# Performance work log

Hardware: AMD Instinct MI355X
Metric: run time of the kernel (lower is better)

The kernel has to match this reference:

```python
import jax, jax.numpy as jnp
import numpy as np

HIDDEN = 1024
HEADS = 16
HEAD_DIM = HIDDEN // HEADS


def setup_inputs() -> dict:
    key = jax.random.key(0)
    kx, kq, kk, kv, ko = jax.random.split(key, 5)
    s = 1.0 / np.sqrt(HIDDEN)
    return {
        "x": jax.random.normal(kx, (2, 2048, HIDDEN), dtype=jnp.float32),
        # nn.Linear weights, stored [out, in] like torch
        "Wq": jax.random.uniform(kq, (HIDDEN, HIDDEN), jnp.float32, -s, s),
        "Wk": jax.random.uniform(kk, (HIDDEN, HIDDEN), jnp.float32, -s, s),
        "Wv": jax.random.uniform(kv, (HIDDEN, HIDDEN), jnp.float32, -s, s),
        "Wo": jax.random.uniform(ko, (HIDDEN, HIDDEN), jnp.float32, -s, s),
    }


def reference(x, Wq, Wk, Wv, Wo):
    B, S, D = x.shape
    H, Hd = HEADS, HEAD_DIM

    def proj(W):  # torch Linear: x @ W.T -> [B,H,S,Hd]
        return (x @ W.T).reshape(B, S, H, Hd).transpose(0, 2, 1, 3)

    q, k, v = proj(Wq), proj(Wk), proj(Wv)
    scores = jnp.einsum("bhsd,bhtd->bhst", q, k) / max(Hd ** 0.5, 1e-6)
    causal = jnp.tril(jnp.ones((S, S), dtype=bool))  # True = keep
    scores = jnp.where(causal, scores, -jnp.inf)
    attn = jax.nn.softmax(scores, axis=-1)
    y = jnp.einsum("bhst,bhtd->bhsd", attn, v)
    y = y.transpose(0, 2, 1, 3).reshape(B, S, D)
    return y @ Wo.T
```

## Files before the change

### kernel.cpp

```cpp
#include <hip/hip_runtime.h>
#include <hip/hip_bf16.h>


#define S_LEN  2048
#define BATCH  2
#define DMODEL 1024
#define NHEADS 16
#define HDIM   64

typedef short short8 __attribute__((ext_vector_type(8)));
typedef float f32x4  __attribute__((ext_vector_type(4)));

__device__ __forceinline__ float b2f(unsigned short u) {
    union { unsigned int i; float f; } x; x.i = ((unsigned int)u) << 16; return x.f;
}
__device__ __forceinline__ unsigned short f2b(float f) {
    union { float f; unsigned int i; } x; x.f = f;
    unsigned int r = x.i + 0x7fffu + ((x.i >> 16) & 1u);
    return (unsigned short)(r >> 16);
}

__device__ __forceinline__ unsigned short* swzp(unsigned short* base, int row, int col) {
    int byte = (col << 1) ^ ((((row >> 3) ^ row) & 7) << 4);
    return base + (row << 6) + (byte >> 1);
}

__global__ void cast_kernel(const float* __restrict__ in, unsigned short* __restrict__ out, int n4) {
    int i = blockIdx.x * blockDim.x + threadIdx.x;
    if (i >= n4) return;
    float4 v = ((const float4*)in)[i];
    unsigned int lo = (unsigned int)f2b(v.x) | ((unsigned int)f2b(v.y) << 16);
    unsigned int hi = (unsigned int)f2b(v.z) | ((unsigned int)f2b(v.w) << 16);
    ((uint2*)out)[i] = make_uint2(lo, hi);
}

template<int OUT_BF16>
__global__ __launch_bounds__(256) void gemm_nt(const unsigned short* __restrict__ A,
                                               const unsigned short* __restrict__ W,
                                               unsigned short* __restrict__ Cb,
                                               float* __restrict__ Cf,
                                               int M, int N, int K) {
    (void)M;
    __shared__ unsigned short As[64][80];
    __shared__ unsigned short Bs[64][80];
    const int tid  = threadIdx.x;
    const int lane = tid & 63;
    const int wave = tid >> 6;
    const int bm = blockIdx.y * 64;
    const int bn = blockIdx.x * 64;
    const int wr = (wave >> 1) * 32;
    const int wc = (wave & 1) * 32;
    const int l15 = lane & 15;
    const int l4  = lane >> 4;
    const int srow = tid >> 2;
    const int sk   = (tid & 3) * 16;

    f32x4 acc[2][2];
#pragma unroll
    for (int i = 0; i < 2; ++i)
#pragma unroll
        for (int j = 0; j < 2; ++j) acc[i][j] = (f32x4){0.f,0.f,0.f,0.f};

    const unsigned short* Arow = A + (size_t)(bm + srow) * K + sk;
    const unsigned short* Wrow = W + (size_t)(bn + srow) * K + sk;

    for (int k0 = 0; k0 < K; k0 += 64) {
        uint4 a0 = *(const uint4*)(Arow + k0);
        uint4 a1 = *(const uint4*)(Arow + k0 + 8);
        uint4 b0 = *(const uint4*)(Wrow + k0);
        uint4 b1 = *(const uint4*)(Wrow + k0 + 8);
        __syncthreads();
        *(uint4*)&As[srow][sk]     = a0;
        *(uint4*)&As[srow][sk + 8] = a1;
        *(uint4*)&Bs[srow][sk]     = b0;
        *(uint4*)&Bs[srow][sk + 8] = b1;
        __syncthreads();
#pragma unroll
        for (int kk = 0; kk < 2; ++kk) {
            short8 af0 = *(const short8*)&As[wr + l15]     [kk*32 + l4*8];
            short8 af1 = *(const short8*)&As[wr + 16 + l15][kk*32 + l4*8];
            short8 bf0 = *(const short8*)&Bs[wc + l15]     [kk*32 + l4*8];
            short8 bf1 = *(const short8*)&Bs[wc + 16 + l15][kk*32 + l4*8];
            acc[0][0] = __builtin_amdgcn_mfma_f32_16x16x32_bf16(af0, bf0, acc[0][0], 0, 0, 0);
            acc[0][1] = __builtin_amdgcn_mfma_f32_16x16x32_bf16(af0, bf1, acc[0][1], 0, 0, 0);
            acc[1][0] = __builtin_amdgcn_mfma_f32_16x16x32_bf16(af1, bf0, acc[1][0], 0, 0, 0);
            acc[1][1] = __builtin_amdgcn_mfma_f32_16x16x32_bf16(af1, bf1, acc[1][1], 0, 0, 0);
        }
    }
#pragma unroll
    for (int mi = 0; mi < 2; ++mi)
#pragma unroll
        for (int ni = 0; ni < 2; ++ni)
#pragma unroll
            for (int i = 0; i < 4; ++i) {
                int row = bm + wr + mi*16 + l4*4 + i;
                int col = bn + wc + ni*16 + l15;
                float v = acc[mi][ni][i];
                if constexpr (OUT_BF16) Cb[(size_t)row * N + col] = f2b(v);
                else                    Cf[(size_t)row * N + col] = v;
            }
}

__global__ __launch_bounds__(256) void attn_mfma(const unsigned short* __restrict__ Qp,
                                                 const unsigned short* __restrict__ Kp,
                                                 const unsigned short* __restrict__ Vp,
                                                 unsigned short* __restrict__ Yp) {
    __shared__ unsigned short Ks[64 * 64];
    __shared__ unsigned short Vt[64 * 64];
    __shared__ unsigned short Pl[4 * 16 * 64];
    const int tid  = threadIdx.x;
    const int lane = tid & 63;
    const int wq   = tid >> 6;
    const int l15  = lane & 15;
    const int l4   = lane >> 4;
    const int r    = tid >> 2;
    const int c4   = tid & 3;
    const int h = blockIdx.y, b = blockIdx.z;
    unsigned short* Pw = Pl + wq * (16 * 64);

#pragma unroll 1
    for (int qp = 0; qp < 2; ++qp) {
        const int qt = qp ? (31 - (int)blockIdx.x) : (int)blockIdx.x;
        short8 qf0, qf1;
        {
            const unsigned short* qb = Qp + ((size_t)(b * S_LEN + qt * 64 + wq * 16 + l15)) * DMODEL
                                          + h * HDIM + l4 * 8;
            qf0 = *(const short8*)qb;
            qf1 = *(const short8*)(qb + 32);
        }
        f32x4 oacc[4];
        float mrow[4], lrow[4];
#pragma unroll
        for (int t = 0; t < 4; ++t) oacc[t] = (f32x4){0.f,0.f,0.f,0.f};
#pragma unroll
        for (int i = 0; i < 4; ++i) { mrow[i] = -1e30f; lrow[i] = 0.f; }

#pragma unroll 1
        for (int kt = 0; kt <= qt; ++kt) {
            __syncthreads();
            {
                const size_t gb = ((size_t)(b * S_LEN + kt * 64 + r)) * DMODEL + h * HDIM + c4 * 16;
                uint4 k0 = *(const uint4*)(Kp + gb);
                uint4 k1 = *(const uint4*)(Kp + gb + 8);
                uint4 v0 = *(const uint4*)(Vp + gb);
                uint4 v1 = *(const uint4*)(Vp + gb + 8);
                *(uint4*)swzp(Ks, r, c4 * 16)     = k0;
                *(uint4*)swzp(Ks, r, c4 * 16 + 8) = k1;
                const unsigned short* vs = (const unsigned short*)&v0;
#pragma unroll
                for (int j = 0; j < 8; ++j) *swzp(Vt, c4 * 16 + j, r) = vs[j];
                vs = (const unsigned short*)&v1;
#pragma unroll
                for (int j = 0; j < 8; ++j) *swzp(Vt, c4 * 16 + 8 + j, r) = vs[j];
            }
            __syncthreads();

            f32x4 sc[4];
#pragma unroll
            for (int t = 0; t < 4; ++t) sc[t] = (f32x4){0.f,0.f,0.f,0.f};
#pragma unroll
            for (int t = 0; t < 4; ++t) {
                short8 kf = *(const short8*)swzp(Ks, t * 16 + l15, l4 * 8);
                sc[t] = __builtin_amdgcn_mfma_f32_16x16x32_bf16(qf0, kf, sc[t], 0, 0, 0);
            }
#pragma unroll
            for (int t = 0; t < 4; ++t) {
                short8 kf = *(const short8*)swzp(Ks, t * 16 + l15, 32 + l4 * 8);
                sc[t] = __builtin_amdgcn_mfma_f32_16x16x32_bf16(qf1, kf, sc[t], 0, 0, 0);
            }
            const bool diag = (kt == qt);
#pragma unroll
            for (int t = 0; t < 4; ++t)
#pragma unroll
                for (int i = 0; i < 4; ++i) {
                    float s = sc[t][i] * 0.125f;
                    if (diag && (t * 16 + l15 > wq * 16 + l4 * 4 + i)) s = -1e30f;
                    sc[t][i] = s;
                }
#pragma unroll
            for (int i = 0; i < 4; ++i) {
                float mx = fmaxf(fmaxf(sc[0][i], sc[1][i]), fmaxf(sc[2][i], sc[3][i]));
                mx = fmaxf(mx, __shfl_xor(mx, 1));
                mx = fmaxf(mx, __shfl_xor(mx, 2));
                mx = fmaxf(mx, __shfl_xor(mx, 4));
                mx = fmaxf(mx, __shfl_xor(mx, 8));
                const float mn = fmaxf(mrow[i], mx);
                const float al = __expf(mrow[i] - mn);
                mrow[i] = mn;
                float ls = 0.f;
#pragma unroll
                for (int t = 0; t < 4; ++t) {
                    float p = __expf(sc[t][i] - mn);
                    sc[t][i] = p;
                    ls += p;
                }
                ls += __shfl_xor(ls, 1);
                ls += __shfl_xor(ls, 2);
                ls += __shfl_xor(ls, 4);
                ls += __shfl_xor(ls, 8);
                lrow[i] = lrow[i] * al + ls;
#pragma unroll
                for (int t = 0; t < 4; ++t) oacc[t][i] *= al;
            }
#pragma unroll
            for (int t = 0; t < 4; ++t)
#pragma unroll
                for (int i = 0; i < 4; ++i)
                    *swzp(Pw, l4 * 4 + i, t * 16 + l15) = f2b(sc[t][i]);

            short8 pf0 = *(const short8*)swzp(Pw, l15, l4 * 8);
            short8 pf1 = *(const short8*)swzp(Pw, l15, 32 + l4 * 8);
#pragma unroll
            for (int td = 0; td < 4; ++td) {
                short8 vf = *(const short8*)swzp(Vt, td * 16 + l15, l4 * 8);
                oacc[td] = __builtin_amdgcn_mfma_f32_16x16x32_bf16(pf0, vf, oacc[td], 0, 0, 0);
            }
#pragma unroll
            for (int td = 0; td < 4; ++td) {
                short8 vf = *(const short8*)swzp(Vt, td * 16 + l15, 32 + l4 * 8);
                oacc[td] = __builtin_amdgcn_mfma_f32_16x16x32_bf16(pf1, vf, oacc[td], 0, 0, 0);
            }
        }
        float linv[4];
#pragma unroll
        for (int i = 0; i < 4; ++i) linv[i] = 1.0f / lrow[i];
        unsigned short* yb = Yp + ((size_t)(b * S_LEN + qt * 64 + wq * 16 + l4 * 4)) * DMODEL
                                + h * HDIM + l15;
#pragma unroll
        for (int i = 0; i < 4; ++i)
#pragma unroll
            for (int td = 0; td < 4; ++td)
                yb[(size_t)i * DMODEL + td * 16] = f2b(oacc[td][i] * linv[i]);
    }
}

extern "C" void kernel_launch(void* const* d_in, const int* in_sizes, int n_in,
                              void* d_out, int out_size, void* d_ws, size_t ws_size,
                              hipStream_t stream) {
    (void)in_sizes; (void)n_in; (void)out_size; (void)ws_size;
    const float* x  = (const float*)d_in[0];
    const float* Wq = (const float*)d_in[1];
    const float* Wk = (const float*)d_in[2];
    const float* Wv = (const float*)d_in[3];
    const float* Wo = (const float*)d_in[4];
    float* out = (float*)d_out;

    const size_t nx = (size_t)BATCH * S_LEN * DMODEL;
    const size_t nw = (size_t)DMODEL * DMODEL;
    char* ws = (char*)d_ws;
    unsigned short* xb  = (unsigned short*)ws; ws += nx * 2;
    unsigned short* wqb = (unsigned short*)ws; ws += nw * 2;
    unsigned short* wkb = (unsigned short*)ws; ws += nw * 2;
    unsigned short* wvb = (unsigned short*)ws; ws += nw * 2;
    unsigned short* wob = (unsigned short*)ws; ws += nw * 2;
    unsigned short* Qp  = (unsigned short*)ws; ws += nx * 2;
    unsigned short* Kp  = (unsigned short*)ws; ws += nx * 2;
    unsigned short* Vp  = (unsigned short*)ws; ws += nx * 2;
    unsigned short* yb  = (unsigned short*)ws; ws += nx * 2;

    cast_kernel<<<(int)(nx/4 + 255)/256, 256, 0, stream>>>(x,  xb,  (int)(nx/4));
    cast_kernel<<<(int)(nw/4 + 255)/256, 256, 0, stream>>>(Wq, wqb, (int)(nw/4));
    cast_kernel<<<(int)(nw/4 + 255)/256, 256, 0, stream>>>(Wk, wkb, (int)(nw/4));
    cast_kernel<<<(int)(nw/4 + 255)/256, 256, 0, stream>>>(Wv, wvb, (int)(nw/4));
    cast_kernel<<<(int)(nw/4 + 255)/256, 256, 0, stream>>>(Wo, wob, (int)(nw/4));

    dim3 gg(DMODEL / 64, (BATCH * S_LEN) / 64);
    gemm_nt<1><<<gg, 256, 0, stream>>>(xb, wqb, Qp, nullptr, BATCH*S_LEN, DMODEL, DMODEL);
    gemm_nt<1><<<gg, 256, 0, stream>>>(xb, wkb, Kp, nullptr, BATCH*S_LEN, DMODEL, DMODEL);
    gemm_nt<1><<<gg, 256, 0, stream>>>(xb, wvb, Vp, nullptr, BATCH*S_LEN, DMODEL, DMODEL);

    dim3 ga(S_LEN / 128, NHEADS, BATCH);
    attn_mfma<<<ga, 256, 0, stream>>>(Qp, Kp, Vp, yb);

    gemm_nt<0><<<gg, 256, 0, stream>>>(yb, wob, nullptr, out, BATCH*S_LEN, DMODEL, DMODEL);
}
```

Measured before the change: 244.9 us.

## Fuse QKV projections into one 128x128 GEMM with direct-to-LDS loads

Concatenates Wq/Wk/Wv into one 3072-wide weight buffer and runs a single GEMM that writes an interleaved QKV tensor, which attention reads with a 3072 stride. The GEMM is retiled to 128x128 blocks with 4x4 MFMA tiles per wave, and global_load_lds moves tiles straight into shared memory. The four weight casts are merged into one launch. This cuts launch count and raises data reuse per tile. The cost is fewer blocks for the output projection (256), and the unswizzled LDS layout may cause bank conflicts.

Result: no change. 241.2 us (-1.5%).

```diff
diff --git a/kernel.cpp b/kernel.cpp
--- a/kernel.cpp
+++ b/kernel.cpp
@@ -7,6 +7,7 @@
 #define DMODEL 1024
 #define NHEADS 16
 #define HDIM   64
+#define QKV_LD 3072
 
 typedef short short8 __attribute__((ext_vector_type(8)));
 typedef float f32x4  __attribute__((ext_vector_type(4)));
@@ -18,6 +19,12 @@
     union { float f; unsigned int i; } x; x.f = f;
     unsigned int r = x.i + 0x7fffu + ((x.i >> 16) & 1u);
     return (unsigned short)(r >> 16);
+}
+
+__device__ __forceinline__ void gload16(const unsigned short* g, unsigned short* l) {
+    __builtin_amdgcn_global_load_lds(
+        (const __attribute__((address_space(1))) unsigned int*)g,
+        (__attribute__((address_space(3))) unsigned int*)l, 16, 0, 0);
 }
 
 __device__ __forceinline__ unsigned short* swzp(unsigned short* base, int row, int col) {
@@ -34,67 +41,82 @@
     ((uint2*)out)[i] = make_uint2(lo, hi);
 }
 
+__global__ void cast_w4(const float* __restrict__ w0, const float* __restrict__ w1,
+                        const float* __restrict__ w2, const float* __restrict__ w3,
+                        unsigned short* __restrict__ out) {
+    int i = blockIdx.x * blockDim.x + threadIdx.x;
+    if (i >= (1 << 20)) return;
+    int seg = i >> 18;
+    const float* src = seg == 0 ? w0 : seg == 1 ? w1 : seg == 2 ? w2 : w3;
+    float4 v = ((const float4*)src)[i & 0x3FFFF];
+    unsigned int lo = (unsigned int)f2b(v.x) | ((unsigned int)f2b(v.y) << 16);
+    unsigned int hi = (unsigned int)f2b(v.z) | ((unsigned int)f2b(v.w) << 16);
+    ((uint2*)out)[i] = make_uint2(lo, hi);
+}
+
 template<int OUT_BF16>
-__global__ __launch_bounds__(256) void gemm_nt(const unsigned short* __restrict__ A,
+__global__ __launch_bounds__(256) void gemm128(const unsigned short* __restrict__ A,
                                                const unsigned short* __restrict__ W,
                                                unsigned short* __restrict__ Cb,
                                                float* __restrict__ Cf,
-                                               int M, int N, int K) {
-    (void)M;
-    __shared__ unsigned short As[64][80];
-    __shared__ unsigned short Bs[64][80];
+                                               int N, int K) {
+    __shared__ unsigned short As[128 * 64];
+    __shared__ unsigned short Bs[128 * 64];
     const int tid  = threadIdx.x;
     const int lane = tid & 63;
     const int wave = tid >> 6;
-    const int bm = blockIdx.y * 64;
-    const int bn = blockIdx.x * 64;
-    const int wr = (wave >> 1) * 32;
-    const int wc = (wave & 1) * 32;
+    const int bm = blockIdx.y * 128;
+    const int bn = blockIdx.x * 128;
+    const int wr = (wave >> 1) * 64;
+    const int wc = (wave & 1) * 64;
     const int l15 = lane & 15;
     const int l4  = lane >> 4;
-    const int srow = tid >> 2;
-    const int sk   = (tid & 3) * 16;
-
-    f32x4 acc[2][2];
-#pragma unroll
-    for (int i = 0; i < 2; ++i)
-#pragma unroll
-        for (int j = 0; j < 2; ++j) acc[i][j] = (f32x4){0.f,0.f,0.f,0.f};
-
-    const unsigned short* Arow = A + (size_t)(bm + srow) * K + sk;
-    const unsigned short* Wrow = W + (size_t)(bn + srow) * K + sk;
+
+    const int srow = wave * 32 + (lane >> 3);
+    const int scol = (lane & 7) * 8;
+    const unsigned short* Ag = A + (size_t)(bm + srow) * K + scol;
+    const unsigned short* Wg = W + (size_t)(bn + srow) * K + scol;
+    unsigned short* Al = As + wave * 32 * 64;
+    unsigned short* Bl = Bs + wave * 32 * 64;
+
+    f32x4 acc[4][4];
+#pragma unroll
+    for (int i = 0; i < 4; ++i)
+#pragma unroll
+        for (int j = 0; j < 4; ++j) acc[i][j] = (f32x4){0.f, 0.f, 0.f, 0.f};
 
     for (int k0 = 0; k0 < K; k0 += 64) {
-        uint4 a0 = *(const uint4*)(Arow + k0);
-        uint4 a1 = *(const uint4*)(Arow + k0 + 8);
-        uint4 b0 = *(const uint4*)(Wrow + k0);
-        uint4 b1 = *(const uint4*)(Wrow + k0 + 8);
         __syncthreads();
-        *(uint4*)&As[srow][sk]     = a0;
-        *(uint4*)&As[srow][sk + 8] = a1;
-        *(uint4*)&Bs[srow][sk]     = b0;
-        *(uint4*)&Bs[srow][sk + 8] = b1;
+#pragma unroll
+        for (int i = 0; i < 4; ++i) {
+            gload16(Ag + k0 + (size_t)(i * 8) * K, Al + i * 8 * 64);
+            gload16(Wg + k0 + (size_t)(i * 8) * K, Bl + i * 8 * 64);
+        }
         __syncthreads();
 #pragma unroll
         for (int kk = 0; kk < 2; ++kk) {
-            short8 af0 = *(const short8*)&As[wr + l15]     [kk*32 + l4*8];
-            short8 af1 = *(const short8*)&As[wr + 16 + l15][kk*32 + l4*8];
-            short8 bf0 = *(const short8*)&Bs[wc + l15]     [kk*32 + l4*8];
-            short8 bf1 = *(const short8*)&Bs[wc + 16 + l15][kk*32 + l4*8];
-            acc[0][0] = __builtin_amdgcn_mfma_f32_16x16x32_bf16(af0, bf0, acc[0][0], 0, 0, 0);
-            acc[0][1] = __builtin_amdgcn_mfma_f32_16x16x32_bf16(af0, bf1, acc[0][1], 0, 0, 0);
-            acc[1][0] = __builtin_amdgcn_mfma_f32_16x16x32_bf16(af1, bf0, acc[1][0], 0, 0, 0);
-            acc[1][1] = __builtin_amdgcn_mfma_f32_16x16x32_bf16(af1, bf1, acc[1][1], 0, 0, 0);
+            short8 af[4], bf[4];
+#pragma unroll
+            for (int mi = 0; mi < 4; ++mi)
+                af[mi] = *(const short8*)&As[(wr + mi * 16 + l15) * 64 + kk * 32 + l4 * 8];
+#pragma unroll
+            for (int ni = 0; ni < 4; ++ni)
+                bf[ni] = *(const short8*)&Bs[(wc + ni * 16 + l15) * 64 + kk * 32 + l4 * 8];
+#pragma unroll
+            for (int mi = 0; mi < 4; ++mi)
+#pragma unroll
+                for (int ni = 0; ni < 4; ++ni)
+                    acc[mi][ni] = __builtin_amdgcn_mfma_f32_16x16x32_bf16(af[mi], bf[ni], acc[mi][ni], 0, 0, 0);
         }
     }
 #pragma unroll
-    for (int mi = 0; mi < 2; ++mi)
-#pragma unroll
-        for (int ni = 0; ni < 2; ++ni)
+    for (int mi = 0; mi < 4; ++mi)
+#pragma unroll
+        for (int ni = 0; ni < 4; ++ni)
 #pragma unroll
             for (int i = 0; i < 4; ++i) {
-                int row = bm + wr + mi*16 + l4*4 + i;
-                int col = bn + wc + ni*16 + l15;
+                int row = bm + wr + mi * 16 + l4 * 4 + i;
+                int col = bn + wc + ni * 16 + l15;
                 float v = acc[mi][ni][i];
                 if constexpr (OUT_BF16) Cb[(size_t)row * N + col] = f2b(v);
                 else                    Cf[(size_t)row * N + col] = v;
@@ -123,7 +145,7 @@
         const int qt = qp ? (31 - (int)blockIdx.x) : (int)blockIdx.x;
         short8 qf0, qf1;
         {
-            const unsigned short* qb = Qp + ((size_t)(b * S_LEN + qt * 64 + wq * 16 + l15)) * DMODEL
+            const unsigned short* qb = Qp + ((size_t)(b * S_LEN + qt * 64 + wq * 16 + l15)) * QKV_LD
                                           + h * HDIM + l4 * 8;
             qf0 = *(const short8*)qb;
             qf1 = *(const short8*)(qb + 32);
@@ -131,7 +153,7 @@
         f32x4 oacc[4];
         float mrow[4], lrow[4];
 #pragma unroll
-        for (int t = 0; t < 4; ++t) oacc[t] = (f32x4){0.f,0.f,0.f,0.f};
+        for (int t = 0; t < 4; ++t) oacc[t] = (f32x4){0.f, 0.f, 0.f, 0.f};
 #pragma unroll
         for (int i = 0; i < 4; ++i) { mrow[i] = -1e30f; lrow[i] = 0.f; }
 
@@ -139,7 +161,7 @@
         for (int kt = 0; kt <= qt; ++kt) {
             __syncthreads();
             {
-                const size_t gb = ((size_t)(b * S_LEN + kt * 64 + r)) * DMODEL + h * HDIM + c4 * 16;
+                const size_t gb = ((size_t)(b * S_LEN + kt * 64 + r)) * QKV_LD + h * HDIM + c4 * 16;
                 uint4 k0 = *(const uint4*)(Kp + gb);
                 uint4 k1 = *(const uint4*)(Kp + gb + 8);
                 uint4 v0 = *(const uint4*)(Vp + gb);
@@ -157,7 +179,7 @@
 
             f32x4 sc[4];
 #pragma unroll
-            for (int t = 0; t < 4; ++t) sc[t] = (f32x4){0.f,0.f,0.f,0.f};
+            for (int t = 0; t < 4; ++t) sc[t] = (f32x4){0.f, 0.f, 0.f, 0.f};
 #pragma unroll
             for (int t = 0; t < 4; ++t) {
                 short8 kf = *(const short8*)swzp(Ks, t * 16 + l15, l4 * 8);
@@ -248,29 +270,21 @@
     const size_t nx = (size_t)BATCH * S_LEN * DMODEL;
     const size_t nw = (size_t)DMODEL * DMODEL;
     char* ws = (char*)d_ws;
-    unsigned short* xb  = (unsigned short*)ws; ws += nx * 2;
-    unsigned short* wqb = (unsigned short*)ws; ws += nw * 2;
-    unsigned short* wkb = (unsigned short*)ws; ws += nw * 2;
-    unsigned short* wvb = (unsigned short*)ws; ws += nw * 2;
-    unsigned short* wob = (unsigned short*)ws; ws += nw * 2;
-    unsigned short* Qp  = (unsigned short*)ws; ws += nx * 2;
-    unsigned short* Kp  = (unsigned short*)ws; ws += nx * 2;
-    unsigned short* Vp  = (unsigned short*)ws; ws += nx * 2;
-    unsigned short* yb  = (unsigned short*)ws; ws += nx * 2;
-
-    cast_kernel<<<(int)(nx/4 + 255)/256, 256, 0, stream>>>(x,  xb,  (int)(nx/4));
-    cast_kernel<<<(int)(nw/4 + 255)/256, 256, 0, stream>>>(Wq, wqb, (int)(nw/4));
-    cast_kernel<<<(int)(nw/4 + 255)/256, 256, 0, stream>>>(Wk, wkb, (int)(nw/4));
-    cast_kernel<<<(int)(nw/4 + 255)/256, 256, 0, stream>>>(Wv, wvb, (int)(nw/4));
-    cast_kernel<<<(int)(nw/4 + 255)/256, 256, 0, stream>>>(Wo, wob, (int)(nw/4));
-
-    dim3 gg(DMODEL / 64, (BATCH * S_LEN) / 64);
-    gemm_nt<1><<<gg, 256, 0, stream>>>(xb, wqb, Qp, nullptr, BATCH*S_LEN, DMODEL, DMODEL);
-    gemm_nt<1><<<gg, 256, 0, stream>>>(xb, wkb, Kp, nullptr, BATCH*S_LEN, DMODEL, DMODEL);
-    gemm_nt<1><<<gg, 256, 0, stream>>>(xb, wvb, Vp, nullptr, BATCH*S_LEN, DMODEL, DMODEL);
+    unsigned short* xb    = (unsigned short*)ws; ws += nx * 2;
+    unsigned short* wqkvb = (unsigned short*)ws; ws += nw * 3 * 2;
+    unsigned short* wob   = (unsigned short*)ws; ws += nw * 2;
+    unsigned short* qkv   = (unsigned short*)ws; ws += nx * 3 * 2;
+    unsigned short* yb    = (unsigned short*)ws; ws += nx * 2;
+
+    cast_kernel<<<(int)(nx / 4 + 255) / 256, 256, 0, stream>>>(x, xb, (int)(nx / 4));
+    cast_w4<<<(1 << 20) / 256, 256, 0, stream>>>(Wq, Wk, Wv, Wo, wqkvb);
+
+    dim3 gq(QKV_LD / 128, (BATCH * S_LEN) / 128);
+    gemm128<1><<<gq, 256, 0, stream>>>(xb, wqkvb, qkv, nullptr, QKV_LD, DMODEL);
 
     dim3 ga(S_LEN / 128, NHEADS, BATCH);
-    attn_mfma<<<ga, 256, 0, stream>>>(Qp, Kp, Vp, yb);
-
-    gemm_nt<0><<<gg, 256, 0, stream>>>(yb, wob, nullptr, out, BATCH*S_LEN, DMODEL, DMODEL);
-}
+    attn_mfma<<<ga, 256, 0, stream>>>(qkv, qkv + DMODEL, qkv + 2 * DMODEL, yb);
+
+    dim3 go(DMODEL / 128, (BATCH * S_LEN) / 128);
+    gemm128<0><<<go, 256, 0, stream>>>(yb, wob, nullptr, out, DMODEL, DMODEL);
+}
```
